# Optimization experiments

Measured on AMD Instinct MI355X. Metric: run time of the kernel, lower is better.

## Reference

```python
import jax, jax.numpy as jnp
import numpy as np

D_MODEL = 1024
NUM_HEADS = 16
D_K = D_MODEL // NUM_HEADS  # 64
B, S = 4, 1024


def setup_inputs() -> dict:
    key = jax.random.key(0)
    ks = jax.random.split(key, 8)
    scale = 1.0 / np.sqrt(D_MODEL)
    return {
        "query": jax.random.normal(ks[0], (B, S, D_MODEL), dtype=jnp.float32),
        "key": jax.random.normal(ks[1], (B, S, D_MODEL), dtype=jnp.float32),
        "value": jax.random.normal(ks[2], (B, S, D_MODEL), dtype=jnp.float32),
        "mask": jnp.ones((B, S, S), dtype=jnp.int32),
        # per-head projection weights, stacked: [H, d_model, d_k]
        "Wq": jax.random.normal(ks[3], (NUM_HEADS, D_MODEL, D_K), dtype=jnp.float32) * scale,
        "Wk": jax.random.normal(ks[4], (NUM_HEADS, D_MODEL, D_K), dtype=jnp.float32) * scale,
        "Wv": jax.random.normal(ks[5], (NUM_HEADS, D_MODEL, D_K), dtype=jnp.float32) * scale,
        # out projection: [H*d_v, d_model]
        "Wo": jax.random.normal(ks[6], (NUM_HEADS * D_K, D_MODEL), dtype=jnp.float32) * scale,
    }


def reference(query, key, value, mask, Wq, Wk, Wv, Wo):
    H, _, d_k = Wq.shape
    b, s, _ = query.shape
    inv_sqrt_dk = 1.0 / np.sqrt(d_k).astype(np.float32)
    # per-head projections (vectorized over heads): [H, B, S, d_k]
    q = jnp.einsum("bsd,hdk->hbsk", query, Wq)
    k = jnp.einsum("bsd,hdk->hbsk", key, Wk)
    v = jnp.einsum("bsd,hdk->hbsk", value, Wv)
    # raw scores before masking are what the torch module returns as q_key_dots
    scores = jnp.einsum("hbqk,hbmk->hbqm", q, k) * inv_sqrt_dk  # [H,B,Sq,Sk]
    masked = jnp.where(mask[None, :, :, :] == 0, -jnp.inf, scores)
    p_attn = jax.nn.softmax(masked, axis=-1)
    attn_out = jnp.einsum("hbqm,hbmk->hbqk", p_attn, v)  # [H,B,S,d_k]
    # concat heads along last dim in head order (matches torch.cat over h)
    concat = jnp.transpose(attn_out, (1, 2, 0, 3)).reshape(b, s, H * d_k)
    out = concat @ Wo  # [B,S,d_model]
    # torch returns (out, list of per-head masked scores); stack as [H,B,S,S]
    return out, masked
```

## Files before the change

kernel.cpp:

```cpp
#include <hip/hip_runtime.h>
#include <hip/hip_bf16.h>
#include <math.h>

typedef __attribute__((ext_vector_type(8))) short short8;
typedef __attribute__((ext_vector_type(4))) float f32x4;


static __device__ __forceinline__ unsigned short f2bf(float x) {
  union { float f; unsigned u; } v; v.f = x;
  unsigned r = v.u + 0x7fffu + ((v.u >> 16) & 1u);
  return (unsigned short)(r >> 16);
}

static __device__ __forceinline__ void bar_lds() {
  asm volatile("s_waitcnt lgkmcnt(0)" ::: "memory");
  __builtin_amdgcn_s_barrier();
}

__global__ __launch_bounds__(256) void prep_wt(
    const float* __restrict__ Wq, const float* __restrict__ Wk,
    const float* __restrict__ Wv, unsigned short* __restrict__ wt) {
  int idx = blockIdx.x * 256 + threadIdx.x;
  int which = idx >> 18;
  int rem = idx & 262143;
  int h = rem >> 14;
  int d = (rem >> 4) & 1023;
  int n4 = rem & 15;
  const float* W = which == 0 ? Wq : (which == 1 ? Wk : Wv);
  float4 v = *(const float4*)(W + (size_t)h * 65536 + (size_t)d * 64 + n4 * 4);
  unsigned short* dst = wt + (size_t)which * 1048576 + ((size_t)h * 64 + n4 * 4) * 1024 + d;
  dst[0]    = f2bf(v.x);
  dst[1024] = f2bf(v.y);
  dst[2048] = f2bf(v.z);
  dst[3072] = f2bf(v.w);
}

__global__ __launch_bounds__(256) void proj_kernel(
    const float* __restrict__ q_in, const float* __restrict__ k_in,
    const float* __restrict__ v_in, const unsigned short* __restrict__ wt,
    unsigned short* __restrict__ qws, unsigned short* __restrict__ kws,
    unsigned short* __restrict__ vws) {
  __shared__ unsigned short lds[(64 + 256) * 72];
  unsigned short* Xs = lds;
  unsigned short* Ws = lds + 64 * 72;
  const int tid = threadIdx.x;
  const int s0 = blockIdx.x * 64;
  const int hg = blockIdx.y;
  const int b = blockIdx.z & 3;
  const int which = blockIdx.z >> 2;
  const float* X = which == 0 ? q_in : (which == 1 ? k_in : v_in);
  const unsigned short* wbase = wt + (size_t)which * 1048576 + (size_t)hg * 256 * 1024;
  const int w = tid >> 6, lane = tid & 63, q16 = lane & 15, quad = lane >> 4;

  f32x4 acc[4][4];
  #pragma unroll
  for (int m = 0; m < 4; ++m)
    #pragma unroll
    for (int j = 0; j < 4; ++j) acc[m][j] = (f32x4)0.0f;

  for (int kt = 0; kt < 16; ++kt) {
    #pragma unroll
    for (int p = 0; p < 4; ++p) {
      int idx = tid + p * 256;
      int r = idx >> 4, c4 = idx & 15;
      const float4 v = *(const float4*)(X + (size_t)(b * 1024 + s0 + r) * 1024 + kt * 64 + c4 * 4);
      ushort4 u;
      u.x = f2bf(v.x); u.y = f2bf(v.y); u.z = f2bf(v.z); u.w = f2bf(v.w);
      *(ushort4*)&Xs[r * 72 + c4 * 4] = u;
    }
    #pragma unroll
    for (int p = 0; p < 8; ++p) {
      int idx = tid + p * 256;
      int r = idx >> 3, c = idx & 7;
      *(uint4*)&Ws[r * 72 + c * 8] = *(const uint4*)(wbase + (size_t)r * 1024 + kt * 64 + c * 8);
    }
    __syncthreads();
    #pragma unroll
    for (int kk = 0; kk < 2; ++kk) {
      short8 a[4];
      #pragma unroll
      for (int m = 0; m < 4; ++m)
        a[m] = *(const short8*)&Xs[(m * 16 + q16) * 72 + kk * 32 + quad * 8];
      #pragma unroll
      for (int j = 0; j < 4; ++j) {
        short8 bb = *(const short8*)&Ws[(w * 64 + j * 16 + q16) * 72 + kk * 32 + quad * 8];
        #pragma unroll
        for (int m = 0; m < 4; ++m)
          acc[m][j] = __builtin_amdgcn_mfma_f32_16x16x32_bf16(a[m], bb, acc[m][j], 0, 0, 0);
      }
    }
    __syncthreads();
  }

  if (which != 2) {
    unsigned short* Cs = lds;
    #pragma unroll
    for (int m = 0; m < 4; ++m)
      #pragma unroll
      for (int j = 0; j < 4; ++j)
        #pragma unroll
        for (int r = 0; r < 4; ++r)
          Cs[(m * 16 + quad * 4 + r) * 264 + w * 64 + j * 16 + q16] = f2bf(acc[m][j][r]);
    __syncthreads();
    unsigned short* dst = which ? kws : qws;
    #pragma unroll
    for (int p = 0; p < 8; ++p) {
      int idx = tid + p * 256;
      int sl = idx >> 5, t = idx & 31;
      int nl = t * 8;
      int head = hg * 4 + (nl >> 6), ko = nl & 63;
      *(uint4*)(dst + ((size_t)((b * 16 + head) * 1024 + s0 + sl)) * 64 + ko) =
          *(const uint4*)&Cs[sl * 264 + nl];
    }
  } else {
    unsigned short* Cs = lds;
    #pragma unroll
    for (int m = 0; m < 4; ++m)
      #pragma unroll
      for (int j = 0; j < 4; ++j)
        #pragma unroll
        for (int r = 0; r < 4; ++r)
          Cs[(w * 64 + j * 16 + q16) * 72 + m * 16 + quad * 4 + r] = f2bf(acc[m][j][r]);
    __syncthreads();
    #pragma unroll
    for (int p = 0; p < 8; ++p) {
      int idx = tid + p * 256;
      int nl = idx >> 3, c = idx & 7;
      int head = hg * 4 + (nl >> 6), d = nl & 63;
      *(uint4*)(vws + ((size_t)((b * 16 + head) * 64 + d)) * 1024 + s0 + c * 8) =
          *(const uint4*)&Cs[nl * 72 + c * 8];
    }
  }
}

__global__ __launch_bounds__(256) void attn_kernel(
    const unsigned short* __restrict__ qws, const unsigned short* __restrict__ kws,
    const unsigned short* __restrict__ vws, const int* __restrict__ mask,
    float* __restrict__ scores, unsigned short* __restrict__ cws) {
  __shared__ unsigned short Qs[64 * 72];
  __shared__ unsigned short Ks[64 * 72];
  __shared__ unsigned short Vts[64 * 72];
  __shared__ unsigned short Ps[64 * 72];
  const int tid = threadIdx.x;
  const int q0 = blockIdx.x * 64;
  const int h = blockIdx.y;
  const int b = blockIdx.z;
  const int w = tid >> 6, lane = tid & 63, q16 = lane & 15, quad = lane >> 4;
  const size_t bh = (size_t)(b * 16 + h);

  const int r1 = tid >> 3, c1 = tid & 7;
  const int r2 = (tid + 256) >> 3;
  const unsigned short* ksrc0 = kws + bh * 1024 * 64;
  const unsigned short* vsrc0 = vws + bh * 64 * 1024;

  {
    const unsigned short* src = qws + (bh * 1024 + q0) * 64;
    *(uint4*)&Qs[r1 * 72 + c1 * 8] = *(const uint4*)(src + r1 * 64 + c1 * 8);
    *(uint4*)&Qs[r2 * 72 + c1 * 8] = *(const uint4*)(src + r2 * 64 + c1 * 8);
  }
  uint4 kr0 = *(const uint4*)(ksrc0 + r1 * 64 + c1 * 8);
  uint4 kr1 = *(const uint4*)(ksrc0 + r2 * 64 + c1 * 8);
  uint4 vr0 = *(const uint4*)(vsrc0 + (size_t)r1 * 1024 + c1 * 8);
  uint4 vr1 = *(const uint4*)(vsrc0 + (size_t)r2 * 1024 + c1 * 8);

  bar_lds();
  short8 aq0 = *(const short8*)&Qs[(w * 16 + q16) * 72 + quad * 8];
  short8 aq1 = *(const short8*)&Qs[(w * 16 + q16) * 72 + 32 + quad * 8];

  f32x4 o[4];
  #pragma unroll
  for (int j = 0; j < 4; ++j) o[j] = (f32x4)0.0f;
  float m_run[4] = {-3.0e38f, -3.0e38f, -3.0e38f, -3.0e38f};
  float l_run[4] = {0.f, 0.f, 0.f, 0.f};

  for (int kt = 0; kt < 16; ++kt) {
    *(uint4*)&Ks[r1 * 72 + c1 * 8] = kr0;
    *(uint4*)&Ks[r2 * 72 + c1 * 8] = kr1;
    *(uint4*)&Vts[r1 * 72 + c1 * 8] = vr0;
    *(uint4*)&Vts[r2 * 72 + c1 * 8] = vr1;
    if (kt < 15) {
      const unsigned short* ksrc = ksrc0 + (size_t)(kt + 1) * 64 * 64;
      const unsigned short* vsrc = vsrc0 + (kt + 1) * 64;
      kr0 = *(const uint4*)(ksrc + r1 * 64 + c1 * 8);
      kr1 = *(const uint4*)(ksrc + r2 * 64 + c1 * 8);
      vr0 = *(const uint4*)(vsrc + (size_t)r1 * 1024 + c1 * 8);
      vr1 = *(const uint4*)(vsrc + (size_t)r2 * 1024 + c1 * 8);
    }
    bar_lds();

    f32x4 sacc[4];
    #pragma unroll
    for (int j = 0; j < 4; ++j) sacc[j] = (f32x4)0.0f;
    #pragma unroll
    for (int j = 0; j < 4; ++j) {
      short8 bb = *(const short8*)&Ks[(j * 16 + q16) * 72 + quad * 8];
      sacc[j] = __builtin_amdgcn_mfma_f32_16x16x32_bf16(aq0, bb, sacc[j], 0, 0, 0);
    }
    #pragma unroll
    for (int j = 0; j < 4; ++j) {
      short8 bb = *(const short8*)&Ks[(j * 16 + q16) * 72 + 32 + quad * 8];
      sacc[j] = __builtin_amdgcn_mfma_f32_16x16x32_bf16(aq1, bb, sacc[j], 0, 0, 0);
    }

    float rm[4] = {-3.0e38f, -3.0e38f, -3.0e38f, -3.0e38f};
    #pragma unroll
    for (int j = 0; j < 4; ++j) {
      #pragma unroll
      for (int r = 0; r < 4; ++r) {
        int ql = w * 16 + quad * 4 + r;
        int q = q0 + ql;
        int key = kt * 64 + j * 16 + q16;
        int mk = mask[((size_t)b * 1024 + q) * 1024 + key];
        float sv = sacc[j][r] * 0.125f;
        scores[(((size_t)h * 4 + b) * 1024 + q) * 1024 + key] = mk ? sv : -INFINITY;
        sv = mk ? sv : -3.0e38f;
        sacc[j][r] = sv;
        rm[r] = fmaxf(rm[r], sv);
      }
    }
    #pragma unroll
    for (int mM = 1; mM <= 8; mM <<= 1) {
      #pragma unroll
      for (int r = 0; r < 4; ++r) rm[r] = fmaxf(rm[r], __shfl_xor(rm[r], mM));
    }
    float rs[4];
    #pragma unroll
    for (int r = 0; r < 4; ++r) {
      float mnew = fmaxf(m_run[r], rm[r]);
      float alpha = __expf(m_run[r] - mnew);
      m_run[r] = mnew;
      l_run[r] *= alpha;
      #pragma unroll
      for (int j = 0; j < 4; ++j) o[j][r] *= alpha;
      rs[r] = 0.f;
    }
    #pragma unroll
    for (int j = 0; j < 4; ++j) {
      #pragma unroll
      for (int r = 0; r < 4; ++r) {
        float p = __expf(sacc[j][r] - m_run[r]);
        rs[r] += p;
        int ql = w * 16 + quad * 4 + r;
        Ps[ql * 72 + j * 16 + q16] = f2bf(p);
      }
    }
    #pragma unroll
    for (int mM = 1; mM <= 8; mM <<= 1) {
      #pragma unroll
      for (int r = 0; r < 4; ++r) rs[r] += __shfl_xor(rs[r], mM);
    }
    #pragma unroll
    for (int r = 0; r < 4; ++r) l_run[r] += rs[r];

    #pragma unroll
    for (int kk = 0; kk < 2; ++kk) {
      short8 a = *(const short8*)&Ps[(w * 16 + q16) * 72 + kk * 32 + quad * 8];
      #pragma unroll
      for (int j = 0; j < 4; ++j) {
        short8 bb = *(const short8*)&Vts[(j * 16 + q16) * 72 + kk * 32 + quad * 8];
        o[j] = __builtin_amdgcn_mfma_f32_16x16x32_bf16(a, bb, o[j], 0, 0, 0);
      }
    }
    bar_lds();
  }

  float inv[4];
  #pragma unroll
  for (int r = 0; r < 4; ++r) inv[r] = 1.0f / l_run[r];
  #pragma unroll
  for (int j = 0; j < 4; ++j) {
    #pragma unroll
    for (int r = 0; r < 4; ++r) {
      int ql = w * 16 + quad * 4 + r;
      int d = j * 16 + q16;
      cws[((size_t)(b * 1024 + q0 + ql)) * 1024 + h * 64 + d] = f2bf(o[j][r] * inv[r]);
    }
  }
}

__global__ __launch_bounds__(256) void outproj_kernel(
    const unsigned short* __restrict__ cws, const float* __restrict__ Wo,
    float* __restrict__ out) {
  __shared__ unsigned short As[64 * 72];
  __shared__ unsigned short Bs[64 * 72];
  const int tid = threadIdx.x;
  const int m0 = blockIdx.x * 64;
  const int n0 = blockIdx.y * 64;
  const int w = tid >> 6, lane = tid & 63, q16 = lane & 15, quad = lane >> 4;
  f32x4 acc[4];
  #pragma unroll
  for (int j = 0; j < 4; ++j) acc[j] = (f32x4)0.0f;

  for (int kt = 0; kt < 16; ++kt) {
    #pragma unroll
    for (int p = 0; p < 2; ++p) {
      int idx = tid + p * 256, r = idx >> 3, c = idx & 7;
      *(uint4*)&As[r * 72 + c * 8] = *(const uint4*)(cws + (size_t)(m0 + r) * 1024 + kt * 64 + c * 8);
    }
    #pragma unroll
    for (int p = 0; p < 16; ++p) {
      int kr = p * 4 + (tid >> 6);
      int n = tid & 63;
      Bs[n * 72 + kr] = f2bf(Wo[(size_t)(kt * 64 + kr) * 1024 + n0 + n]);
    }
    __syncthreads();
    #pragma unroll
    for (int kk = 0; kk < 2; ++kk) {
      short8 a = *(const short8*)&As[(w * 16 + q16) * 72 + kk * 32 + quad * 8];
      #pragma unroll
      for (int j = 0; j < 4; ++j) {
        short8 bb = *(const short8*)&Bs[(j * 16 + q16) * 72 + kk * 32 + quad * 8];
        acc[j] = __builtin_amdgcn_mfma_f32_16x16x32_bf16(a, bb, acc[j], 0, 0, 0);
      }
    }
    __syncthreads();
  }
  #pragma unroll
  for (int j = 0; j < 4; ++j) {
    #pragma unroll
    for (int r = 0; r < 4; ++r) {
      out[(size_t)(m0 + w * 16 + quad * 4 + r) * 1024 + n0 + j * 16 + q16] = acc[j][r];
    }
  }
}

extern "C" void kernel_launch(void* const* d_in, const int* in_sizes, int n_in,
                              void* d_out, int out_size, void* d_ws, size_t ws_size,
                              hipStream_t stream) {
  (void)in_sizes; (void)n_in; (void)out_size; (void)ws_size;
  const float* q_in = (const float*)d_in[0];
  const float* k_in = (const float*)d_in[1];
  const float* v_in = (const float*)d_in[2];
  const int* mask   = (const int*)d_in[3];
  const float* Wq   = (const float*)d_in[4];
  const float* Wk   = (const float*)d_in[5];
  const float* Wv   = (const float*)d_in[6];
  const float* Wo   = (const float*)d_in[7];

  float* out = (float*)d_out;
  float* scores = out + (size_t)4 * 1024 * 1024;

  unsigned short* qws = (unsigned short*)d_ws;
  unsigned short* kws = qws + (size_t)4 * 16 * 1024 * 64;
  unsigned short* vws = kws + (size_t)4 * 16 * 1024 * 64;
  unsigned short* cws = vws + (size_t)4 * 16 * 1024 * 64;
  unsigned short* wt  = cws;

  prep_wt<<<dim3(3072), 256, 0, stream>>>(Wq, Wk, Wv, wt);
  proj_kernel<<<dim3(16, 4, 12), 256, 0, stream>>>(q_in, k_in, v_in, wt, qws, kws, vws);
  attn_kernel<<<dim3(16, 16, 4), 256, 0, stream>>>(qws, kws, vws, mask, scores, cws);
  outproj_kernel<<<dim3(64, 16), 256, 0, stream>>>(cws, Wo, out);
}
```

Measured before the change: 535.9 us.

## Pretranspose Wo to bf16, remap attention grid for XCD locality, lazy rescale

Result: faster. 519.4 us, median of 2 (-3.1%).

```diff
diff --git a/kernel.cpp b/kernel.cpp
--- a/kernel.cpp
+++ b/kernel.cpp
@@ -19,20 +19,33 @@
 
 __global__ __launch_bounds__(256) void prep_wt(
     const float* __restrict__ Wq, const float* __restrict__ Wk,
-    const float* __restrict__ Wv, unsigned short* __restrict__ wt) {
-  int idx = blockIdx.x * 256 + threadIdx.x;
-  int which = idx >> 18;
-  int rem = idx & 262143;
-  int h = rem >> 14;
-  int d = (rem >> 4) & 1023;
-  int n4 = rem & 15;
-  const float* W = which == 0 ? Wq : (which == 1 ? Wk : Wv);
-  float4 v = *(const float4*)(W + (size_t)h * 65536 + (size_t)d * 64 + n4 * 4);
-  unsigned short* dst = wt + (size_t)which * 1048576 + ((size_t)h * 64 + n4 * 4) * 1024 + d;
-  dst[0]    = f2bf(v.x);
-  dst[1024] = f2bf(v.y);
-  dst[2048] = f2bf(v.z);
-  dst[3072] = f2bf(v.w);
+    const float* __restrict__ Wv, const float* __restrict__ Wo,
+    unsigned short* __restrict__ wt, unsigned short* __restrict__ wot) {
+  if (blockIdx.x < 3072) {
+    int idx = blockIdx.x * 256 + threadIdx.x;
+    int which = idx >> 18;
+    int rem = idx & 262143;
+    int h = rem >> 14;
+    int d = (rem >> 4) & 1023;
+    int n4 = rem & 15;
+    const float* W = which == 0 ? Wq : (which == 1 ? Wk : Wv);
+    float4 v = *(const float4*)(W + (size_t)h * 65536 + (size_t)d * 64 + n4 * 4);
+    unsigned short* dst = wt + (size_t)which * 1048576 + ((size_t)h * 64 + n4 * 4) * 1024 + d;
+    dst[0]    = f2bf(v.x);
+    dst[1024] = f2bf(v.y);
+    dst[2048] = f2bf(v.z);
+    dst[3072] = f2bf(v.w);
+  } else {
+    int idx = (blockIdx.x - 3072) * 256 + threadIdx.x;
+    int k = idx >> 8;
+    int n4 = idx & 255;
+    float4 v = *(const float4*)(Wo + (size_t)k * 1024 + n4 * 4);
+    unsigned short* dst = wot + ((size_t)n4 * 4) * 1024 + k;
+    dst[0]    = f2bf(v.x);
+    dst[1024] = f2bf(v.y);
+    dst[2048] = f2bf(v.z);
+    dst[3072] = f2bf(v.w);
+  }
 }
 
 __global__ __launch_bounds__(256) void proj_kernel(
@@ -142,9 +155,12 @@
   __shared__ unsigned short Vts[64 * 72];
   __shared__ unsigned short Ps[64 * 72];
   const int tid = threadIdx.x;
-  const int q0 = blockIdx.x * 64;
-  const int h = blockIdx.y;
-  const int b = blockIdx.z;
+  const int L = blockIdx.x;
+  const int xcd = L & 7, t = L >> 3;
+  const int h = (((t >> 3) & 3) << 2) | (xcd & 3);
+  const int qt = ((t & 7) << 1) | (xcd >> 2);
+  const int b = t >> 5;
+  const int q0 = qt * 64;
   const int w = tid >> 6, lane = tid & 63, q16 = lane & 15, quad = lane >> 4;
   const size_t bh = (size_t)(b * 16 + h);
 
@@ -223,17 +239,21 @@
       #pragma unroll
       for (int r = 0; r < 4; ++r) rm[r] = fmaxf(rm[r], __shfl_xor(rm[r], mM));
     }
-    float rs[4];
-    #pragma unroll
-    for (int r = 0; r < 4; ++r) {
-      float mnew = fmaxf(m_run[r], rm[r]);
-      float alpha = __expf(m_run[r] - mnew);
-      m_run[r] = mnew;
-      l_run[r] *= alpha;
-      #pragma unroll
-      for (int j = 0; j < 4; ++j) o[j][r] *= alpha;
-      rs[r] = 0.f;
-    }
+    int need = 0;
+    #pragma unroll
+    for (int r = 0; r < 4; ++r) need |= (rm[r] > m_run[r] + 8.0f);
+    if (__any(need)) {
+      #pragma unroll
+      for (int r = 0; r < 4; ++r) {
+        float mnew = fmaxf(m_run[r], rm[r]);
+        float alpha = __expf(m_run[r] - mnew);
+        m_run[r] = mnew;
+        l_run[r] *= alpha;
+        #pragma unroll
+        for (int j = 0; j < 4; ++j) o[j][r] *= alpha;
+      }
+    }
+    float rs[4] = {0.f, 0.f, 0.f, 0.f};
     #pragma unroll
     for (int j = 0; j < 4; ++j) {
       #pragma unroll
@@ -279,7 +299,7 @@
 }
 
 __global__ __launch_bounds__(256) void outproj_kernel(
-    const unsigned short* __restrict__ cws, const float* __restrict__ Wo,
+    const unsigned short* __restrict__ cws, const unsigned short* __restrict__ wot,
     float* __restrict__ out) {
   __shared__ unsigned short As[64 * 72];
   __shared__ unsigned short Bs[64 * 72];
@@ -296,12 +316,7 @@
     for (int p = 0; p < 2; ++p) {
       int idx = tid + p * 256, r = idx >> 3, c = idx & 7;
       *(uint4*)&As[r * 72 + c * 8] = *(const uint4*)(cws + (size_t)(m0 + r) * 1024 + kt * 64 + c * 8);
-    }
-    #pragma unroll
-    for (int p = 0; p < 16; ++p) {
-      int kr = p * 4 + (tid >> 6);
-      int n = tid & 63;
-      Bs[n * 72 + kr] = f2bf(Wo[(size_t)(kt * 64 + kr) * 1024 + n0 + n]);
+      *(uint4*)&Bs[r * 72 + c * 8] = *(const uint4*)(wot + (size_t)(n0 + r) * 1024 + kt * 64 + c * 8);
     }
     __syncthreads();
     #pragma unroll
@@ -345,9 +360,10 @@
   unsigned short* vws = kws + (size_t)4 * 16 * 1024 * 64;
   unsigned short* cws = vws + (size_t)4 * 16 * 1024 * 64;
   unsigned short* wt  = cws;
-
-  prep_wt<<<dim3(3072), 256, 0, stream>>>(Wq, Wk, Wv, wt);
+  unsigned short* wot = cws + (size_t)4 * 1024 * 1024;
+
+  prep_wt<<<dim3(4096), 256, 0, stream>>>(Wq, Wk, Wv, Wo, wt, wot);
   proj_kernel<<<dim3(16, 4, 12), 256, 0, stream>>>(q_in, k_in, v_in, wt, qws, kws, vws);
-  attn_kernel<<<dim3(16, 16, 4), 256, 0, stream>>>(qws, kws, vws, mask, scores, cws);
-  outproj_kernel<<<dim3(64, 16), 256, 0, stream>>>(cws, Wo, out);
-}
+  attn_kernel<<<dim3(1024), 256, 0, stream>>>(qws, kws, vws, mask, scores, cws);
+  outproj_kernel<<<dim3(64, 16), 256, 0, stream>>>(cws, wot, out);
+}
```
